# Optimization experiments

Measured on AMD Instinct MI355X. Metric: run time of the kernel, lower is better.

Reference implementation:

```python
import jax, jax.numpy as jnp
import numpy as np

N = 50000      # nodes
E = 600000     # edges
H = 128        # hidden_features (= in_features)
ED = 16        # edge_attr_dim
B = 256        # number of graphs in batch
L = 5          # num_layers
OUT = 128      # out_features


def _xavier(key, shape):
    fan_in, fan_out = shape
    a = float(np.sqrt(6.0 / (fan_in + fan_out)))
    return jax.random.uniform(key, shape, jnp.float32, -a, a)


def setup_inputs() -> dict:
    key = jax.random.key(0)
    ks = jax.random.split(key, 32)
    x = jax.random.normal(ks[0], (N, H), jnp.float32)
    edge_index = jax.random.randint(ks[1], (2, E), 0, N, jnp.int32)
    edge_attr = jax.random.normal(ks[2], (E, ED), jnp.float32)
    batch = jnp.sort(jax.random.randint(ks[3], (N,), 0, B, jnp.int32))
    # per-layer parameters, stacked along leading L axis (in=hidden so uniform)
    node_W = jnp.stack([_xavier(jax.random.fold_in(ks[4], i), (H, H)) for i in range(L)])
    edge_W = jnp.stack([_xavier(jax.random.fold_in(ks[5], i), (ED, H)) for i in range(L)])
    mlp1_W = jnp.stack([_xavier(jax.random.fold_in(ks[6], i), (H, H)) for i in range(L)])
    mlp2_W = jnp.stack([_xavier(jax.random.fold_in(ks[7], i), (H, H)) for i in range(L)])
    zb = jnp.zeros((L, H), jnp.float32)
    # virtual-node update MLP (shared across layers) and final classifier
    vn_w0 = _xavier(ks[8], (H, H)); vn_b0 = jnp.zeros((H,), jnp.float32)
    vn_w1 = _xavier(ks[9], (H, H)); vn_b1 = jnp.zeros((H,), jnp.float32)
    fc_W = _xavier(ks[10], (H, OUT)); fc_b = jnp.zeros((OUT,), jnp.float32)
    vn_init = jnp.zeros((1, H), jnp.float32)  # embedding initialized to 0
    return {
        "x": x, "edge_attr": edge_attr,
        "node_W": node_W, "node_b": zb, "edge_W": edge_W, "edge_b": zb,
        "mlp1_W": mlp1_W, "mlp1_b": zb, "mlp2_W": mlp2_W, "mlp2_b": zb,
        "vn_w0": vn_w0, "vn_b0": vn_b0, "vn_w1": vn_w1, "vn_b1": vn_b1,
        "fc_W": fc_W, "fc_b": fc_b, "vn_init": vn_init,
        "edge_index": edge_index, "batch": batch,
    }


def reference(x, edge_attr, node_W, node_b, edge_W, edge_b, mlp1_W, mlp1_b,
              mlp2_W, mlp2_b, vn_w0, vn_b0, vn_w1, vn_b1, fc_W, fc_b,
              vn_init, edge_index, batch):
    src, dst = edge_index[0], edge_index[1]
    # per-graph node counts for mean pooling (guard against empty graphs)
    counts = jnp.maximum(
        jax.ops.segment_sum(jnp.ones((N, 1), x.dtype), batch, num_segments=B), 1.0)
    vn = jnp.broadcast_to(vn_init, (B, H))  # weight.repeat(batch_size, 1)

    def layer(carry, p):
        xc, vn = carry
        nW, nb, eW, eb, m1W, m1b, m2W, m2b = p
        h = xc @ nW + nb + vn[batch]              # node encode + VN broadcast
        ea = edge_attr @ eW + eb                   # edge encode [E,H]
        msg = h[src] + ea                          # gather + add
        agg = jax.ops.segment_sum(msg, dst, num_segments=N)  # scatter-add
        out = jax.nn.relu(agg @ m1W + m1b) @ m2W + m2b        # layer MLP
        xn = jax.nn.relu(out)
        pooled = jax.ops.segment_sum(xn, batch, num_segments=B) / counts
        vn2 = vn + jax.nn.relu(jax.nn.relu(pooled @ vn_w0 + vn_b0) @ vn_w1 + vn_b1)
        return (xn, vn2), None

    (xf, _), _ = jax.lax.scan(
        layer, (x, vn),
        (node_W, node_b, edge_W, edge_b, mlp1_W, mlp1_b, mlp2_W, mlp2_b))
    pooled = jax.ops.segment_sum(xf, batch, num_segments=B) / counts
    return pooled @ fc_W + fc_b
```

## Files before the change

### kernel.cpp

```cpp
#include <hip/hip_runtime.h>

#define NN 50000
#define EE 600000
#define HH 128
#define EDD 16
#define BB 256
#define LL 5
#define NN16 (NN * 16)

typedef float f32x4 __attribute__((ext_vector_type(4)));
typedef _Float16 f16x4 __attribute__((ext_vector_type(4)));
typedef _Float16 f16x8 __attribute__((ext_vector_type(8)));

__global__ __launch_bounds__(256) void wprep_k(const float* __restrict__ W,
    _Float16* __restrict__ Wh, _Float16* __restrict__ Wl, int total)
{
    int idx = blockIdx.x * 256 + threadIdx.x;
    if (idx >= total) return;
    int mat = idx >> 14;
    int r = idx & 16383;
    int j = r & 7, lane = (r >> 3) & 63, ks = (r >> 9) & 3, ntw = (r >> 11) & 7;
    int lm = lane & 15, quad = lane >> 4;
    int n = (ntw >> 1) * 32 + (ntw & 1) * 16 + lm;
    int k = ks * 32 + quad * 8 + j;
    float w = W[(mat << 14) + (k << 7) + n];
    _Float16 h = (_Float16)w;
    Wh[idx] = h;
    Wl[idx] = (_Float16)(w - (float)h);
}

__global__ __launch_bounds__(256) void xprep_k(const float* __restrict__ x,
    _Float16* __restrict__ X)
{
    int i = blockIdx.x * 256 + threadIdx.x;
    if (i >= NN * 32) return;
    float4 v = ((const float4*)x)[i];
    f16x4 o;
    o[0] = (_Float16)v.x; o[1] = (_Float16)v.y; o[2] = (_Float16)v.z; o[3] = (_Float16)v.w;
    ((f16x4*)X)[i] = o;
}

__device__ __forceinline__ void stage_A16(const _Float16* __restrict__ Ag, int M, int brow,
    int tid, _Float16* __restrict__ As)
{
    const int r = tid >> 2, cg = tid & 3;
    const int grow = brow + r;
    _Float16* p = As + r * 136 + cg * 32;
    if (grow < M) {
        const f16x8* s = (const f16x8*)(Ag + (size_t)grow * 128 + cg * 32);
#pragma unroll
        for (int i = 0; i < 4; ++i) ((f16x8*)p)[i] = s[i];
    } else {
        f16x8 z = (f16x8)(_Float16)0;
#pragma unroll
        for (int i = 0; i < 4; ++i) ((f16x8*)p)[i] = z;
    }
}

__device__ __forceinline__ void mfma_stage16(
    const _Float16* __restrict__ As,
    const _Float16* __restrict__ Wh, const _Float16* __restrict__ Wl,
    int wn, int lm, int quad, int lane, f32x4 acc[4][2])
{
    f16x8 Bh[2][4], Bl[2][4];
#pragma unroll
    for (int nt = 0; nt < 2; ++nt)
#pragma unroll
        for (int ks = 0; ks < 4; ++ks) {
            int fi = ((((wn * 2 + nt) * 4) + ks) * 64 + lane) * 8;
            Bh[nt][ks] = *(const f16x8*)(Wh + fi);
            Bl[nt][ks] = *(const f16x8*)(Wl + fi);
        }
#pragma unroll
    for (int ks = 0; ks < 4; ++ks) {
        f16x8 a[4];
#pragma unroll
        for (int mt = 0; mt < 4; ++mt) {
            int off = (mt * 16 + lm) * 136 + ks * 32 + quad * 8;
            a[mt] = *(const f16x8*)(As + off);
        }
#pragma unroll
        for (int mt = 0; mt < 4; ++mt)
#pragma unroll
            for (int nt = 0; nt < 2; ++nt) {
                acc[mt][nt] = __builtin_amdgcn_mfma_f32_16x16x32_f16(a[mt], Bh[nt][ks], acc[mt][nt], 0, 0, 0);
                acc[mt][nt] = __builtin_amdgcn_mfma_f32_16x16x32_f16(a[mt], Bl[nt][ks], acc[mt][nt], 0, 0, 0);
            }
    }
}

__device__ __forceinline__ void store_f16(const _Float16* __restrict__ Fo,
    _Float16* __restrict__ out, int M, int brow, int tid)
{
    const int r = tid >> 2, cg = tid & 3;
    const int grow = brow + r;
    if (grow >= M) return;
    const f16x8* src = (const f16x8*)(Fo + r * 136 + cg * 32);
    f16x8* dst = (f16x8*)(out + (size_t)grow * 128 + cg * 32);
#pragma unroll
    for (int i = 0; i < 4; ++i) dst[i] = src[i];
}

__global__ __launch_bounds__(256) void gemm_node_k(
    const _Float16* __restrict__ Ag,
    const _Float16* __restrict__ Wh, const _Float16* __restrict__ Wl,
    const float* __restrict__ bias, _Float16* __restrict__ out, int M,
    const float* __restrict__ vn, const int* __restrict__ batch)
{
    __shared__ __align__(16) _Float16 smem[64 * 136];
    const int tid = threadIdx.x, brow = blockIdx.x * 64;

    stage_A16(Ag, M, brow, tid, smem);
    __syncthreads();

    const int lane = tid & 63, wn = tid >> 6, lm = lane & 15, quad = lane >> 4;
    f32x4 acc[4][2];
#pragma unroll
    for (int mt = 0; mt < 4; ++mt) { acc[mt][0] = (f32x4)(0.f); acc[mt][1] = (f32x4)(0.f); }
    mfma_stage16(smem, Wh, Wl, wn, lm, quad, lane, acc);
    __syncthreads();

    const int colb = wn * 32 + lm;
    const float b0 = bias[colb], b1 = bias[colb + 16];
#pragma unroll
    for (int mt = 0; mt < 4; ++mt) {
#pragma unroll
        for (int r = 0; r < 4; ++r) {
            int trow = mt * 16 + quad * 4 + r;
            int grow = brow + trow;
            int bg = batch[grow < M ? grow : M - 1];
            const float* vrow = vn + (size_t)bg * 128;
            smem[trow * 136 + colb]      = (_Float16)(acc[mt][0][r] + b0 + vrow[colb]);
            smem[trow * 136 + colb + 16] = (_Float16)(acc[mt][1][r] + b1 + vrow[colb + 16]);
        }
    }
    __syncthreads();
    store_f16(smem, out, M, brow, tid);
}

__global__ __launch_bounds__(256) void gemm_mlp_k(
    const _Float16* __restrict__ Ag,
    const _Float16* __restrict__ W1h, const _Float16* __restrict__ W1l, const float* __restrict__ b1,
    const _Float16* __restrict__ W2h, const _Float16* __restrict__ W2l, const float* __restrict__ b2,
    _Float16* __restrict__ X, int M)
{
    __shared__ __align__(16) _Float16 smem[64 * 136];
    const int tid = threadIdx.x, brow = blockIdx.x * 64;

    stage_A16(Ag, M, brow, tid, smem);
    __syncthreads();

    const int lane = tid & 63, wn = tid >> 6, lm = lane & 15, quad = lane >> 4;
    const int colb = wn * 32 + lm;

    f32x4 acc[4][2];
#pragma unroll
    for (int mt = 0; mt < 4; ++mt) { acc[mt][0] = (f32x4)(0.f); acc[mt][1] = (f32x4)(0.f); }
    mfma_stage16(smem, W1h, W1l, wn, lm, quad, lane, acc);
    __syncthreads();

    {
        const float c0 = b1[colb], c1 = b1[colb + 16];
#pragma unroll
        for (int mt = 0; mt < 4; ++mt) {
#pragma unroll
            for (int r = 0; r < 4; ++r) {
                int trow = mt * 16 + quad * 4 + r;
                smem[trow * 136 + colb]      = (_Float16)fmaxf(acc[mt][0][r] + c0, 0.f);
                smem[trow * 136 + colb + 16] = (_Float16)fmaxf(acc[mt][1][r] + c1, 0.f);
            }
        }
    }
    __syncthreads();

#pragma unroll
    for (int mt = 0; mt < 4; ++mt) { acc[mt][0] = (f32x4)(0.f); acc[mt][1] = (f32x4)(0.f); }
    mfma_stage16(smem, W2h, W2l, wn, lm, quad, lane, acc);
    __syncthreads();

    const float d0 = b2[colb], d1 = b2[colb + 16];
#pragma unroll
    for (int mt = 0; mt < 4; ++mt) {
#pragma unroll
        for (int r = 0; r < 4; ++r) {
            int trow = mt * 16 + quad * 4 + r;
            smem[trow * 136 + colb]      = (_Float16)fmaxf(acc[mt][0][r] + d0, 0.f);
            smem[trow * 136 + colb + 16] = (_Float16)fmaxf(acc[mt][1][r] + d1, 0.f);
        }
    }
    __syncthreads();
    store_f16(smem, X, M, brow, tid);
}

__global__ __launch_bounds__(256) void aggregate_k(
    const _Float16* __restrict__ h, const float* __restrict__ aggE,
    const float* __restrict__ eW, const float* __restrict__ eb,
    const int* __restrict__ rowstart, const int* __restrict__ csr_src,
    _Float16* __restrict__ Ag, int n)
{
    __shared__ float eWs[16 * 128];
    __shared__ float ebs[128];
    const int tid = threadIdx.x;
#pragma unroll
    for (int t = 0; t < 2; ++t) {
        int li = (tid + t * 256) * 4;
        *(float4*)(&eWs[li]) = *(const float4*)(eW + li);
    }
    if (tid < 32) *(float4*)(&ebs[tid * 4]) = *(const float4*)(eb + tid * 4);
    __syncthreads();

    const int lane = tid & 31;
    const int node = blockIdx.x * 8 + (tid >> 5);
    if (node >= n) return;
    const int s = rowstart[node], e = rowstart[node + 1];
    const f16x4* h4 = (const f16x4*)h;

    float4 acc = make_float4(0.f, 0.f, 0.f, 0.f);
    int p = s;
    for (; p + 4 <= e; p += 4) {
        int s0 = csr_src[p], s1 = csr_src[p + 1], s2 = csr_src[p + 2], s3 = csr_src[p + 3];
        f16x4 v0 = h4[(size_t)s0 * 32 + lane];
        f16x4 v1 = h4[(size_t)s1 * 32 + lane];
        f16x4 v2 = h4[(size_t)s2 * 32 + lane];
        f16x4 v3 = h4[(size_t)s3 * 32 + lane];
        acc.x += (float)v0[0] + (float)v1[0] + (float)v2[0] + (float)v3[0];
        acc.y += (float)v0[1] + (float)v1[1] + (float)v2[1] + (float)v3[1];
        acc.z += (float)v0[2] + (float)v1[2] + (float)v2[2] + (float)v3[2];
        acc.w += (float)v0[3] + (float)v1[3] + (float)v2[3] + (float)v3[3];
    }
    for (; p < e; ++p) {
        f16x4 v = h4[(size_t)csr_src[p] * 32 + lane];
        acc.x += (float)v[0]; acc.y += (float)v[1]; acc.z += (float)v[2]; acc.w += (float)v[3];
    }

    const float degf = (float)(e - s);
    const float* ae = aggE + (size_t)node * 16;
    const float4 b4 = *(const float4*)(&ebs[lane * 4]);
    float4 et = make_float4(degf * b4.x, degf * b4.y, degf * b4.z, degf * b4.w);
#pragma unroll
    for (int k = 0; k < 16; ++k) {
        float a = ae[k];
        float4 w = *(const float4*)(&eWs[k * 128 + lane * 4]);
        et.x = fmaf(a, w.x, et.x);
        et.y = fmaf(a, w.y, et.y);
        et.z = fmaf(a, w.z, et.z);
        et.w = fmaf(a, w.w, et.w);
    }
    acc.x += et.x; acc.y += et.y; acc.z += et.z; acc.w += et.w;

    f16x4 o;
    o[0] = (_Float16)acc.x; o[1] = (_Float16)acc.y; o[2] = (_Float16)acc.z; o[3] = (_Float16)acc.w;
    ((f16x4*)Ag)[(size_t)node * 32 + lane] = o;
}

__global__ __launch_bounds__(256) void aggE_k(
    const float* __restrict__ eattr, const int* __restrict__ rowstart,
    const int2* __restrict__ csr_pair, float* __restrict__ aggE, int n)
{
    const int lane = threadIdx.x & 15;
    const int node = blockIdx.x * 16 + (threadIdx.x >> 4);
    if (node >= n) return;
    const int s = rowstart[node], e = rowstart[node + 1];
    float acc = 0.f;
    for (int p = s; p < e; ++p)
        acc += eattr[(size_t)csr_pair[p].y * 16 + lane];
    aggE[(size_t)node * 16 + lane] = acc;
}

__global__ __launch_bounds__(128) void poolvn_k(
    const _Float16* __restrict__ X, const int* __restrict__ gstart,
    const float* __restrict__ W0, const float* __restrict__ b0,
    const float* __restrict__ W1, const float* __restrict__ b1,
    float* __restrict__ vn)
{
    __shared__ float4 red[128];
    __shared__ float p[128], q[128];
    const int g = blockIdx.x, t = threadIdx.x;
    const int c = t & 31, rr = t >> 5;
    const int s = gstart[g], e = gstart[g + 1];
    const f16x4* x4 = (const f16x4*)X;
    float4 a = make_float4(0.f, 0.f, 0.f, 0.f);
    for (int i = s + rr; i < e; i += 4) {
        f16x4 v = x4[(size_t)i * 32 + c];
        a.x += (float)v[0]; a.y += (float)v[1]; a.z += (float)v[2]; a.w += (float)v[3];
    }
    red[t] = a;
    __syncthreads();
    if (t < 32) {
        float4 a0 = red[t], a1 = red[t + 32], a2 = red[t + 64], a3 = red[t + 96];
        float cnt = (float)(e - s);
        if (cnt < 1.f) cnt = 1.f;
        float inv = 1.f / cnt;
        float4 o;
        o.x = (a0.x + a1.x + a2.x + a3.x) * inv;
        o.y = (a0.y + a1.y + a2.y + a3.y) * inv;
        o.z = (a0.z + a1.z + a2.z + a3.z) * inv;
        o.w = (a0.w + a1.w + a2.w + a3.w) * inv;
        ((float4*)p)[t] = o;
    }
    __syncthreads();
    float acc0 = b0[t];
    for (int k = 0; k < 128; ++k) acc0 = fmaf(p[k], W0[k * 128 + t], acc0);
    q[t] = fmaxf(acc0, 0.f);
    __syncthreads();
    float acc1 = b1[t];
    for (int k = 0; k < 128; ++k) acc1 = fmaf(q[k], W1[k * 128 + t], acc1);
    vn[g * 128 + t] += fmaxf(acc1, 0.f);
}

__global__ __launch_bounds__(128) void poolfc_k(
    const _Float16* __restrict__ X, const int* __restrict__ gstart,
    const float* __restrict__ W, const float* __restrict__ b,
    float* __restrict__ out)
{
    __shared__ float4 red[128];
    __shared__ float p[128];
    const int g = blockIdx.x, t = threadIdx.x;
    const int c = t & 31, rr = t >> 5;
    const int s = gstart[g], e = gstart[g + 1];
    const f16x4* x4 = (const f16x4*)X;
    float4 a = make_float4(0.f, 0.f, 0.f, 0.f);
    for (int i = s + rr; i < e; i += 4) {
        f16x4 v = x4[(size_t)i * 32 + c];
        a.x += (float)v[0]; a.y += (float)v[1]; a.z += (float)v[2]; a.w += (float)v[3];
    }
    red[t] = a;
    __syncthreads();
    if (t < 32) {
        float4 a0 = red[t], a1 = red[t + 32], a2 = red[t + 64], a3 = red[t + 96];
        float cnt = (float)(e - s);
        if (cnt < 1.f) cnt = 1.f;
        float inv = 1.f / cnt;
        float4 o;
        o.x = (a0.x + a1.x + a2.x + a3.x) * inv;
        o.y = (a0.y + a1.y + a2.y + a3.y) * inv;
        o.z = (a0.z + a1.z + a2.z + a3.z) * inv;
        o.w = (a0.w + a1.w + a2.w + a3.w) * inv;
        ((float4*)p)[t] = o;
    }
    __syncthreads();
    float acc = b[t];
    for (int k = 0; k < 128; ++k) acc = fmaf(p[k], W[k * 128 + t], acc);
    out[g * 128 + t] = acc;
}

__global__ void histp_k(const int* __restrict__ idx, int n, int* __restrict__ cntp)
{
    int i = blockIdx.x * 256 + threadIdx.x;
    if (i < n) atomicAdd(&cntp[(blockIdx.x & 3) * NN16 + (idx[i] << 4)], 1);
}

__global__ void scan_deg_k(const int* __restrict__ degp, int n, int* __restrict__ out, int* __restrict__ bsum)
{
    __shared__ int s[256];
    int gid = blockIdx.x * 256 + threadIdx.x;
    int v = 0;
    if (gid < n) {
        int o = gid << 4;
        v = degp[o] + degp[NN16 + o] + degp[2 * NN16 + o] + degp[3 * NN16 + o];
    }
    s[threadIdx.x] = v;
    __syncthreads();
    for (int off = 1; off < 256; off <<= 1) {
        int t = (threadIdx.x >= off) ? s[threadIdx.x - off] : 0;
        __syncthreads();
        s[threadIdx.x] += t;
        __syncthreads();
    }
    int incl = s[threadIdx.x];
    if (gid < n) out[gid] = incl - v;
    if (bsum != nullptr && threadIdx.x == 255) bsum[blockIdx.x] = incl;
}

__global__ void scan_k(const int* __restrict__ in, int n, int* __restrict__ out, int* __restrict__ bsum)
{
    __shared__ int s[256];
    int gid = blockIdx.x * 256 + threadIdx.x;
    int v = (gid < n) ? in[gid] : 0;
    s[threadIdx.x] = v;
    __syncthreads();
    for (int off = 1; off < 256; off <<= 1) {
        int t = (threadIdx.x >= off) ? s[threadIdx.x - off] : 0;
        __syncthreads();
        s[threadIdx.x] += t;
        __syncthreads();
    }
    int incl = s[threadIdx.x];
    if (gid < n) out[gid] = incl - v;
    if (bsum != nullptr && threadIdx.x == 255) bsum[blockIdx.x] = incl;
}

__global__ void addoff_k(int* __restrict__ data, const int* __restrict__ boff, int n, int total)
{
    int i = blockIdx.x * 256 + threadIdx.x;
    if (i < n) data[i] += boff[blockIdx.x];
    if (i == 0) data[n] = total;
}

__global__ void curinit_k(const int* __restrict__ rowstart, int* __restrict__ cursorp)
{
    int i = blockIdx.x * 256 + threadIdx.x;
    if (i < NN) cursorp[i << 4] = rowstart[i];
}

__global__ void fill_k(const int* __restrict__ dst, const int* __restrict__ src, int n,
                       int* __restrict__ cursorp, int2* __restrict__ csr_pair)
{
    int e = blockIdx.x * 256 + threadIdx.x;
    if (e < n) {
        int slot = atomicAdd(&cursorp[dst[e] << 4], 1);
        int2 pr; pr.x = src[e]; pr.y = e;
        csr_pair[slot] = pr;
    }
}

__global__ void split_k(const int2* __restrict__ csr_pair, int* __restrict__ csr_src, int n)
{
    int i = blockIdx.x * 256 + threadIdx.x;
    if (i < n) csr_src[i] = csr_pair[i].x;
}

__global__ void gstart_k(const int* __restrict__ batch, int* __restrict__ gstart)
{
    int b = blockIdx.x * 64 + threadIdx.x;
    if (b > BB) return;
    if (b == BB) { gstart[BB] = NN; return; }
    int lo = 0, hi = NN;
    while (lo < hi) {
        int mid = (lo + hi) >> 1;
        if (batch[mid] < b) lo = mid + 1; else hi = mid;
    }
    gstart[b] = lo;
}

__global__ void vninit_k(const float* __restrict__ vninit, float* __restrict__ vn)
{
    int i = blockIdx.x * 256 + threadIdx.x;
    vn[i] = vninit[i & 127];
}

extern "C" void kernel_launch(void* const* d_in, const int* in_sizes, int n_in,
                              void* d_out, int out_size, void* d_ws, size_t ws_size,
                              hipStream_t stream)
{
    (void)in_sizes; (void)n_in; (void)out_size; (void)ws_size;
    const float* x       = (const float*)d_in[0];
    const float* eattr   = (const float*)d_in[1];
    const float* node_W  = (const float*)d_in[2];
    const float* node_b  = (const float*)d_in[3];
    const float* edge_W  = (const float*)d_in[4];
    const float* edge_b  = (const float*)d_in[5];
    const float* mlp1_W  = (const float*)d_in[6];
    const float* mlp1_b  = (const float*)d_in[7];
    const float* mlp2_W  = (const float*)d_in[8];
    const float* mlp2_b  = (const float*)d_in[9];
    const float* vn_w0   = (const float*)d_in[10];
    const float* vn_b0   = (const float*)d_in[11];
    const float* vn_w1   = (const float*)d_in[12];
    const float* vn_b1   = (const float*)d_in[13];
    const float* fc_W    = (const float*)d_in[14];
    const float* fc_b    = (const float*)d_in[15];
    const float* vn_init = (const float*)d_in[16];
    const int*   eidx    = (const int*)d_in[17];
    const int*   batch   = (const int*)d_in[18];
    const int* srcv = eidx;
    const int* dstv = eidx + EE;

    char* wp = (char*)d_ws;
    auto alloc = [&](size_t bytes) -> void* {
        void* p = (void*)wp;
        wp += (bytes + 255) & ~(size_t)255;
        return p;
    };
    _Float16* X0  = (_Float16*)alloc((size_t)NN * HH * 2);
    _Float16* X   = (_Float16*)alloc((size_t)NN * HH * 2);
    _Float16* Ag  = (_Float16*)alloc((size_t)NN * HH * 2);
    _Float16* h16 = (_Float16*)alloc((size_t)NN * HH * 2);
    float* aggE   = (float*)alloc((size_t)NN * EDD * 4);
    float* vn     = (float*)alloc((size_t)BB * HH * 4);
    int* degp     = (int*)alloc((size_t)4 * NN16 * 4);
    int* rowstart = (int*)alloc((size_t)(NN + 1) * 4);
    int* cursorp  = (int*)alloc((size_t)NN16 * 4);
    int2* csr_pair= (int2*)alloc((size_t)EE * 8);
    int* csr_src  = (int*)alloc((size_t)EE * 4);
    int* bsum     = (int*)alloc(256 * 4);
    int* boff     = (int*)alloc(256 * 4);
    int* gstart   = (int*)alloc((size_t)(BB + 1) * 4);
    _Float16* WtN_h = (_Float16*)alloc((size_t)5 * 16384 * 2);
    _Float16* WtN_l = (_Float16*)alloc((size_t)5 * 16384 * 2);
    _Float16* Wt1_h = (_Float16*)alloc((size_t)5 * 16384 * 2);
    _Float16* Wt1_l = (_Float16*)alloc((size_t)5 * 16384 * 2);
    _Float16* Wt2_h = (_Float16*)alloc((size_t)5 * 16384 * 2);
    _Float16* Wt2_l = (_Float16*)alloc((size_t)5 * 16384 * 2);

    hipMemsetAsync(degp, 0, (size_t)4 * NN16 * 4, stream);

    histp_k<<<(EE + 255) / 256, 256, 0, stream>>>(dstv, EE, degp);

    const int NB1 = (NN + 255) / 256;
    scan_deg_k<<<NB1, 256, 0, stream>>>(degp, NN, rowstart, bsum);
    scan_k<<<1, 256, 0, stream>>>(bsum, NB1, boff, nullptr);
    addoff_k<<<NB1, 256, 0, stream>>>(rowstart, boff, NN, EE);
    curinit_k<<<NB1, 256, 0, stream>>>(rowstart, cursorp);
    fill_k<<<(EE + 255) / 256, 256, 0, stream>>>(dstv, srcv, EE, cursorp, csr_pair);
    split_k<<<(EE + 255) / 256, 256, 0, stream>>>(csr_pair, csr_src, EE);

    gstart_k<<<5, 64, 0, stream>>>(batch, gstart);

    aggE_k<<<(NN + 15) / 16, 256, 0, stream>>>(eattr, rowstart, csr_pair, aggE, NN);
    vninit_k<<<(BB * HH) / 256, 256, 0, stream>>>(vn_init, vn);
    xprep_k<<<(NN * 32 + 255) / 256, 256, 0, stream>>>(x, X0);

    wprep_k<<<(5 * 16384 + 255) / 256, 256, 0, stream>>>(node_W, WtN_h, WtN_l, 5 * 16384);
    wprep_k<<<(5 * 16384 + 255) / 256, 256, 0, stream>>>(mlp1_W, Wt1_h, Wt1_l, 5 * 16384);
    wprep_k<<<(5 * 16384 + 255) / 256, 256, 0, stream>>>(mlp2_W, Wt2_h, Wt2_l, 5 * 16384);

    const int GN = (NN + 63) / 64;
    const _Float16* xin = X0;
    for (int l = 0; l < LL; ++l) {
        gemm_node_k<<<GN, 256, 0, stream>>>(xin,
                                            WtN_h + (size_t)l * 16384, WtN_l + (size_t)l * 16384,
                                            node_b + (size_t)l * HH, h16, NN, vn, batch);
        aggregate_k<<<(NN + 7) / 8, 256, 0, stream>>>(h16, aggE, edge_W + (size_t)l * EDD * HH,
                                                      edge_b + (size_t)l * HH, rowstart, csr_src, Ag, NN);
        gemm_mlp_k<<<GN, 256, 0, stream>>>(Ag,
                                           Wt1_h + (size_t)l * 16384, Wt1_l + (size_t)l * 16384, mlp1_b + (size_t)l * HH,
                                           Wt2_h + (size_t)l * 16384, Wt2_l + (size_t)l * 16384, mlp2_b + (size_t)l * HH,
                                           X, NN);
        poolvn_k<<<BB, 128, 0, stream>>>(X, gstart, vn_w0, vn_b0, vn_w1, vn_b1, vn);
        xin = X;
    }
    poolfc_k<<<BB, 128, 0, stream>>>(X, gstart, fc_W, fc_b, (float*)d_out);
}
```

Before: 638.4 us.

## Fuse neighbor aggregation into MLP GEMM and pool via atomics in epilogue

Aggregation of gathered neighbor features and edge terms is now done per 64-row tile directly into shared memory, followed by both MLP GEMMs in the same kernel, eliminating the intermediate Ag buffer. Graph mean-pooling is accumulated via segmented atomicAdd in the epilogue, replacing the separate pooling pass over X, and the final layer's unused VN update is skipped. This reduces global memory traffic and kernel launches but lowers grid parallelism for the latency-bound gather and adds atomic contention plus fp32 nondeterminism in pooling.

Measured after the change: 788.8 us. 1.24x slower.

```diff
diff --git a/kernel.cpp b/kernel.cpp
--- a/kernel.cpp
+++ b/kernel.cpp
@@ -138,69 +138,20 @@
     store_f16(smem, out, M, brow, tid);
 }
 
-__global__ __launch_bounds__(256) void gemm_mlp_k(
-    const _Float16* __restrict__ Ag,
-    const _Float16* __restrict__ W1h, const _Float16* __restrict__ W1l, const float* __restrict__ b1,
-    const _Float16* __restrict__ W2h, const _Float16* __restrict__ W2l, const float* __restrict__ b2,
-    _Float16* __restrict__ X, int M)
-{
-    __shared__ __align__(16) _Float16 smem[64 * 136];
-    const int tid = threadIdx.x, brow = blockIdx.x * 64;
-
-    stage_A16(Ag, M, brow, tid, smem);
-    __syncthreads();
-
-    const int lane = tid & 63, wn = tid >> 6, lm = lane & 15, quad = lane >> 4;
-    const int colb = wn * 32 + lm;
-
-    f32x4 acc[4][2];
-#pragma unroll
-    for (int mt = 0; mt < 4; ++mt) { acc[mt][0] = (f32x4)(0.f); acc[mt][1] = (f32x4)(0.f); }
-    mfma_stage16(smem, W1h, W1l, wn, lm, quad, lane, acc);
-    __syncthreads();
-
-    {
-        const float c0 = b1[colb], c1 = b1[colb + 16];
-#pragma unroll
-        for (int mt = 0; mt < 4; ++mt) {
-#pragma unroll
-            for (int r = 0; r < 4; ++r) {
-                int trow = mt * 16 + quad * 4 + r;
-                smem[trow * 136 + colb]      = (_Float16)fmaxf(acc[mt][0][r] + c0, 0.f);
-                smem[trow * 136 + colb + 16] = (_Float16)fmaxf(acc[mt][1][r] + c1, 0.f);
-            }
-        }
-    }
-    __syncthreads();
-
-#pragma unroll
-    for (int mt = 0; mt < 4; ++mt) { acc[mt][0] = (f32x4)(0.f); acc[mt][1] = (f32x4)(0.f); }
-    mfma_stage16(smem, W2h, W2l, wn, lm, quad, lane, acc);
-    __syncthreads();
-
-    const float d0 = b2[colb], d1 = b2[colb + 16];
-#pragma unroll
-    for (int mt = 0; mt < 4; ++mt) {
-#pragma unroll
-        for (int r = 0; r < 4; ++r) {
-            int trow = mt * 16 + quad * 4 + r;
-            smem[trow * 136 + colb]      = (_Float16)fmaxf(acc[mt][0][r] + d0, 0.f);
-            smem[trow * 136 + colb + 16] = (_Float16)fmaxf(acc[mt][1][r] + d1, 0.f);
-        }
-    }
-    __syncthreads();
-    store_f16(smem, X, M, brow, tid);
-}
-
-__global__ __launch_bounds__(256) void aggregate_k(
+__global__ __launch_bounds__(256) void agg_mlp_k(
     const _Float16* __restrict__ h, const float* __restrict__ aggE,
     const float* __restrict__ eW, const float* __restrict__ eb,
     const int* __restrict__ rowstart, const int* __restrict__ csr_src,
-    _Float16* __restrict__ Ag, int n)
-{
+    const _Float16* __restrict__ W1h, const _Float16* __restrict__ W1l, const float* __restrict__ b1,
+    const _Float16* __restrict__ W2h, const _Float16* __restrict__ W2l, const float* __restrict__ b2,
+    _Float16* __restrict__ X, float* __restrict__ pooled,
+    const int* __restrict__ batch, int M)
+{
+    __shared__ __align__(16) _Float16 As[64 * 136];
     __shared__ float eWs[16 * 128];
     __shared__ float ebs[128];
-    const int tid = threadIdx.x;
+    const int tid = threadIdx.x, brow = blockIdx.x * 64;
+
 #pragma unroll
     for (int t = 0; t < 2; ++t) {
         int li = (tid + t * 256) * 4;
@@ -209,48 +160,110 @@
     if (tid < 32) *(float4*)(&ebs[tid * 4]) = *(const float4*)(eb + tid * 4);
     __syncthreads();
 
-    const int lane = tid & 31;
-    const int node = blockIdx.x * 8 + (tid >> 5);
-    if (node >= n) return;
-    const int s = rowstart[node], e = rowstart[node + 1];
-    const f16x4* h4 = (const f16x4*)h;
-
-    float4 acc = make_float4(0.f, 0.f, 0.f, 0.f);
-    int p = s;
-    for (; p + 4 <= e; p += 4) {
-        int s0 = csr_src[p], s1 = csr_src[p + 1], s2 = csr_src[p + 2], s3 = csr_src[p + 3];
-        f16x4 v0 = h4[(size_t)s0 * 32 + lane];
-        f16x4 v1 = h4[(size_t)s1 * 32 + lane];
-        f16x4 v2 = h4[(size_t)s2 * 32 + lane];
-        f16x4 v3 = h4[(size_t)s3 * 32 + lane];
-        acc.x += (float)v0[0] + (float)v1[0] + (float)v2[0] + (float)v3[0];
-        acc.y += (float)v0[1] + (float)v1[1] + (float)v2[1] + (float)v3[1];
-        acc.z += (float)v0[2] + (float)v1[2] + (float)v2[2] + (float)v3[2];
-        acc.w += (float)v0[3] + (float)v1[3] + (float)v2[3] + (float)v3[3];
-    }
-    for (; p < e; ++p) {
-        f16x4 v = h4[(size_t)csr_src[p] * 32 + lane];
-        acc.x += (float)v[0]; acc.y += (float)v[1]; acc.z += (float)v[2]; acc.w += (float)v[3];
-    }
-
-    const float degf = (float)(e - s);
-    const float* ae = aggE + (size_t)node * 16;
-    const float4 b4 = *(const float4*)(&ebs[lane * 4]);
-    float4 et = make_float4(degf * b4.x, degf * b4.y, degf * b4.z, degf * b4.w);
-#pragma unroll
-    for (int k = 0; k < 16; ++k) {
-        float a = ae[k];
-        float4 w = *(const float4*)(&eWs[k * 128 + lane * 4]);
-        et.x = fmaf(a, w.x, et.x);
-        et.y = fmaf(a, w.y, et.y);
-        et.z = fmaf(a, w.z, et.z);
-        et.w = fmaf(a, w.w, et.w);
-    }
-    acc.x += et.x; acc.y += et.y; acc.z += et.z; acc.w += et.w;
-
-    f16x4 o;
-    o[0] = (_Float16)acc.x; o[1] = (_Float16)acc.y; o[2] = (_Float16)acc.z; o[3] = (_Float16)acc.w;
-    ((f16x4*)Ag)[(size_t)node * 32 + lane] = o;
+    {
+        const int lane32 = tid & 31, grp = tid >> 5;
+        const f16x4* h4 = (const f16x4*)h;
+        const float4 b4 = *(const float4*)(&ebs[lane32 * 4]);
+        for (int i = 0; i < 8; ++i) {
+            const int nl = grp * 8 + i;
+            const int node = brow + nl;
+            float4 acc = make_float4(0.f, 0.f, 0.f, 0.f);
+            if (node < M) {
+                const int s = rowstart[node], e = rowstart[node + 1];
+                int p = s;
+                for (; p + 4 <= e; p += 4) {
+                    int s0 = csr_src[p], s1 = csr_src[p + 1], s2 = csr_src[p + 2], s3 = csr_src[p + 3];
+                    f16x4 v0 = h4[(size_t)s0 * 32 + lane32];
+                    f16x4 v1 = h4[(size_t)s1 * 32 + lane32];
+                    f16x4 v2 = h4[(size_t)s2 * 32 + lane32];
+                    f16x4 v3 = h4[(size_t)s3 * 32 + lane32];
+                    acc.x += (float)v0[0] + (float)v1[0] + (float)v2[0] + (float)v3[0];
+                    acc.y += (float)v0[1] + (float)v1[1] + (float)v2[1] + (float)v3[1];
+                    acc.z += (float)v0[2] + (float)v1[2] + (float)v2[2] + (float)v3[2];
+                    acc.w += (float)v0[3] + (float)v1[3] + (float)v2[3] + (float)v3[3];
+                }
+                for (; p < e; ++p) {
+                    f16x4 v = h4[(size_t)csr_src[p] * 32 + lane32];
+                    acc.x += (float)v[0]; acc.y += (float)v[1]; acc.z += (float)v[2]; acc.w += (float)v[3];
+                }
+                const float degf = (float)(e - s);
+                const float* ae = aggE + (size_t)node * 16;
+                float4 et = make_float4(degf * b4.x, degf * b4.y, degf * b4.z, degf * b4.w);
+#pragma unroll
+                for (int k = 0; k < 16; ++k) {
+                    float a = ae[k];
+                    float4 w = *(const float4*)(&eWs[k * 128 + lane32 * 4]);
+                    et.x = fmaf(a, w.x, et.x);
+                    et.y = fmaf(a, w.y, et.y);
+                    et.z = fmaf(a, w.z, et.z);
+                    et.w = fmaf(a, w.w, et.w);
+                }
+                acc.x += et.x; acc.y += et.y; acc.z += et.z; acc.w += et.w;
+            }
+            f16x4 o;
+            o[0] = (_Float16)acc.x; o[1] = (_Float16)acc.y; o[2] = (_Float16)acc.z; o[3] = (_Float16)acc.w;
+            *(f16x4*)(&As[nl * 136 + lane32 * 4]) = o;
+        }
+    }
+    __syncthreads();
+
+    const int lane = tid & 63, wn = tid >> 6, lm = lane & 15, quad = lane >> 4;
+    const int colb = wn * 32 + lm;
+    f32x4 acc[4][2];
+#pragma unroll
+    for (int mt = 0; mt < 4; ++mt) { acc[mt][0] = (f32x4)(0.f); acc[mt][1] = (f32x4)(0.f); }
+    mfma_stage16(As, W1h, W1l, wn, lm, quad, lane, acc);
+    __syncthreads();
+    {
+        const float c0 = b1[colb], c1 = b1[colb + 16];
+#pragma unroll
+        for (int mt = 0; mt < 4; ++mt) {
+#pragma unroll
+            for (int r = 0; r < 4; ++r) {
+                int trow = mt * 16 + quad * 4 + r;
+                As[trow * 136 + colb]      = (_Float16)fmaxf(acc[mt][0][r] + c0, 0.f);
+                As[trow * 136 + colb + 16] = (_Float16)fmaxf(acc[mt][1][r] + c1, 0.f);
+            }
+        }
+    }
+    __syncthreads();
+
+#pragma unroll
+    for (int mt = 0; mt < 4; ++mt) { acc[mt][0] = (f32x4)(0.f); acc[mt][1] = (f32x4)(0.f); }
+    mfma_stage16(As, W2h, W2l, wn, lm, quad, lane, acc);
+    __syncthreads();
+    {
+        const float d0 = b2[colb], d1 = b2[colb + 16];
+#pragma unroll
+        for (int mt = 0; mt < 4; ++mt) {
+#pragma unroll
+            for (int r = 0; r < 4; ++r) {
+                int trow = mt * 16 + quad * 4 + r;
+                As[trow * 136 + colb]      = (_Float16)fmaxf(acc[mt][0][r] + d0, 0.f);
+                As[trow * 136 + colb + 16] = (_Float16)fmaxf(acc[mt][1][r] + d1, 0.f);
+            }
+        }
+    }
+    __syncthreads();
+    store_f16(As, X, M, brow, tid);
+
+    {
+        const int c = tid & 127, half = tid >> 7;
+        const int row0 = half * 32;
+        float sum = 0.f;
+        int curg = -1;
+        for (int r2 = 0; r2 < 32; ++r2) {
+            int grow = brow + row0 + r2;
+            if (grow >= M) break;
+            int g = batch[grow];
+            if (g != curg) {
+                if (curg >= 0) atomicAdd(&pooled[curg * 128 + c], sum);
+                curg = g; sum = 0.f;
+            }
+            sum += (float)As[(row0 + r2) * 136 + c];
+        }
+        if (curg >= 0) atomicAdd(&pooled[curg * 128 + c], sum);
+    }
 }
 
 __global__ __launch_bounds__(256) void aggE_k(
@@ -267,77 +280,38 @@
     aggE[(size_t)node * 16 + lane] = acc;
 }
 
-__global__ __launch_bounds__(128) void poolvn_k(
-    const _Float16* __restrict__ X, const int* __restrict__ gstart,
+__global__ __launch_bounds__(128) void vn_update_k(
+    float* __restrict__ pooled, const int* __restrict__ gstart,
     const float* __restrict__ W0, const float* __restrict__ b0,
     const float* __restrict__ W1, const float* __restrict__ b1,
     float* __restrict__ vn)
 {
-    __shared__ float4 red[128];
     __shared__ float p[128], q[128];
     const int g = blockIdx.x, t = threadIdx.x;
-    const int c = t & 31, rr = t >> 5;
-    const int s = gstart[g], e = gstart[g + 1];
-    const f16x4* x4 = (const f16x4*)X;
-    float4 a = make_float4(0.f, 0.f, 0.f, 0.f);
-    for (int i = s + rr; i < e; i += 4) {
-        f16x4 v = x4[(size_t)i * 32 + c];
-        a.x += (float)v[0]; a.y += (float)v[1]; a.z += (float)v[2]; a.w += (float)v[3];
-    }
-    red[t] = a;
-    __syncthreads();
-    if (t < 32) {
-        float4 a0 = red[t], a1 = red[t + 32], a2 = red[t + 64], a3 = red[t + 96];
-        float cnt = (float)(e - s);
-        if (cnt < 1.f) cnt = 1.f;
-        float inv = 1.f / cnt;
-        float4 o;
-        o.x = (a0.x + a1.x + a2.x + a3.x) * inv;
-        o.y = (a0.y + a1.y + a2.y + a3.y) * inv;
-        o.z = (a0.z + a1.z + a2.z + a3.z) * inv;
-        o.w = (a0.w + a1.w + a2.w + a3.w) * inv;
-        ((float4*)p)[t] = o;
-    }
-    __syncthreads();
-    float acc0 = b0[t];
-    for (int k = 0; k < 128; ++k) acc0 = fmaf(p[k], W0[k * 128 + t], acc0);
-    q[t] = fmaxf(acc0, 0.f);
-    __syncthreads();
-    float acc1 = b1[t];
-    for (int k = 0; k < 128; ++k) acc1 = fmaf(q[k], W1[k * 128 + t], acc1);
-    vn[g * 128 + t] += fmaxf(acc1, 0.f);
-}
-
-__global__ __launch_bounds__(128) void poolfc_k(
-    const _Float16* __restrict__ X, const int* __restrict__ gstart,
+    float cnt = (float)(gstart[g + 1] - gstart[g]);
+    if (cnt < 1.f) cnt = 1.f;
+    p[t] = pooled[g * 128 + t] / cnt;
+    pooled[g * 128 + t] = 0.f;
+    __syncthreads();
+    float a0 = b0[t];
+    for (int k = 0; k < 128; ++k) a0 = fmaf(p[k], W0[k * 128 + t], a0);
+    q[t] = fmaxf(a0, 0.f);
+    __syncthreads();
+    float a1 = b1[t];
+    for (int k = 0; k < 128; ++k) a1 = fmaf(q[k], W1[k * 128 + t], a1);
+    vn[g * 128 + t] += fmaxf(a1, 0.f);
+}
+
+__global__ __launch_bounds__(128) void fc_k(
+    const float* __restrict__ pooled, const int* __restrict__ gstart,
     const float* __restrict__ W, const float* __restrict__ b,
     float* __restrict__ out)
 {
-    __shared__ float4 red[128];
     __shared__ float p[128];
     const int g = blockIdx.x, t = threadIdx.x;
-    const int c = t & 31, rr = t >> 5;
-    const int s = gstart[g], e = gstart[g + 1];
-    const f16x4* x4 = (const f16x4*)X;
-    float4 a = make_float4(0.f, 0.f, 0.f, 0.f);
-    for (int i = s + rr; i < e; i += 4) {
-        f16x4 v = x4[(size_t)i * 32 + c];
-        a.x += (float)v[0]; a.y += (float)v[1]; a.z += (float)v[2]; a.w += (float)v[3];
-    }
-    red[t] = a;
-    __syncthreads();
-    if (t < 32) {
-        float4 a0 = red[t], a1 = red[t + 32], a2 = red[t + 64], a3 = red[t + 96];
-        float cnt = (float)(e - s);
-        if (cnt < 1.f) cnt = 1.f;
-        float inv = 1.f / cnt;
-        float4 o;
-        o.x = (a0.x + a1.x + a2.x + a3.x) * inv;
-        o.y = (a0.y + a1.y + a2.y + a3.y) * inv;
-        o.z = (a0.z + a1.z + a2.z + a3.z) * inv;
-        o.w = (a0.w + a1.w + a2.w + a3.w) * inv;
-        ((float4*)p)[t] = o;
-    }
+    float cnt = (float)(gstart[g + 1] - gstart[g]);
+    if (cnt < 1.f) cnt = 1.f;
+    p[t] = pooled[g * 128 + t] / cnt;
     __syncthreads();
     float acc = b[t];
     for (int k = 0; k < 128; ++k) acc = fmaf(p[k], W[k * 128 + t], acc);
@@ -433,10 +407,11 @@
     gstart[b] = lo;
 }
 
-__global__ void vninit_k(const float* __restrict__ vninit, float* __restrict__ vn)
+__global__ void vninit_k(const float* __restrict__ vninit, float* __restrict__ vn, float* __restrict__ pooled)
 {
     int i = blockIdx.x * 256 + threadIdx.x;
     vn[i] = vninit[i & 127];
+    pooled[i] = 0.f;
 }
 
 extern "C" void kernel_launch(void* const* d_in, const int* in_sizes, int n_in,
@@ -474,10 +449,10 @@
     };
     _Float16* X0  = (_Float16*)alloc((size_t)NN * HH * 2);
     _Float16* X   = (_Float16*)alloc((size_t)NN * HH * 2);
-    _Float16* Ag  = (_Float16*)alloc((size_t)NN * HH * 2);
     _Float16* h16 = (_Float16*)alloc((size_t)NN * HH * 2);
     float* aggE   = (float*)alloc((size_t)NN * EDD * 4);
     float* vn     = (float*)alloc((size_t)BB * HH * 4);
+    float* pooled = (float*)alloc((size_t)BB * HH * 4);
     int* degp     = (int*)alloc((size_t)4 * NN16 * 4);
     int* rowstart = (int*)alloc((size_t)(NN + 1) * 4);
     int* cursorp  = (int*)alloc((size_t)NN16 * 4);
@@ -508,7 +483,7 @@
     gstart_k<<<5, 64, 0, stream>>>(batch, gstart);
 
     aggE_k<<<(NN + 15) / 16, 256, 0, stream>>>(eattr, rowstart, csr_pair, aggE, NN);
-    vninit_k<<<(BB * HH) / 256, 256, 0, stream>>>(vn_init, vn);
+    vninit_k<<<(BB * HH) / 256, 256, 0, stream>>>(vn_init, vn, pooled);
     xprep_k<<<(NN * 32 + 255) / 256, 256, 0, stream>>>(x, X0);
 
     wprep_k<<<(5 * 16384 + 255) / 256, 256, 0, stream>>>(node_W, WtN_h, WtN_l, 5 * 16384);
@@ -521,14 +496,14 @@
         gemm_node_k<<<GN, 256, 0, stream>>>(xin,
                                             WtN_h + (size_t)l * 16384, WtN_l + (size_t)l * 16384,
                                             node_b + (size_t)l * HH, h16, NN, vn, batch);
-        aggregate_k<<<(NN + 7) / 8, 256, 0, stream>>>(h16, aggE, edge_W + (size_t)l * EDD * HH,
-                                                      edge_b + (size_t)l * HH, rowstart, csr_src, Ag, NN);
-        gemm_mlp_k<<<GN, 256, 0, stream>>>(Ag,
-                                           Wt1_h + (size_t)l * 16384, Wt1_l + (size_t)l * 16384, mlp1_b + (size_t)l * HH,
-                                           Wt2_h + (size_t)l * 16384, Wt2_l + (size_t)l * 16384, mlp2_b + (size_t)l * HH,
-                                           X, NN);
-        poolvn_k<<<BB, 128, 0, stream>>>(X, gstart, vn_w0, vn_b0, vn_w1, vn_b1, vn);
+        agg_mlp_k<<<GN, 256, 0, stream>>>(h16, aggE, edge_W + (size_t)l * EDD * HH,
+                                          edge_b + (size_t)l * HH, rowstart, csr_src,
+                                          Wt1_h + (size_t)l * 16384, Wt1_l + (size_t)l * 16384, mlp1_b + (size_t)l * HH,
+                                          Wt2_h + (size_t)l * 16384, Wt2_l + (size_t)l * 16384, mlp2_b + (size_t)l * HH,
+                                          X, pooled, batch, NN);
+        if (l < LL - 1)
+            vn_update_k<<<BB, 128, 0, stream>>>(pooled, gstart, vn_w0, vn_b0, vn_w1, vn_b1, vn);
         xin = X;
     }
-    poolfc_k<<<BB, 128, 0, stream>>>(X, gstart, fc_W, fc_b, (float*)d_out);
-}
+    fc_k<<<BB, 128, 0, stream>>>(pooled, gstart, fc_W, fc_b, (float*)d_out);
+}
```
